# Optimization experiments

Measured on AMD Instinct MI355X. Metric: run time of the kernel, lower is better.

Reference implementation:

```python
import jax, jax.numpy as jnp
import numpy as np

B, T, IN, OUT = 131072, 8, 128, 128


def setup_inputs() -> dict:
    key = jax.random.key(0)
    k1, k2, k3, k4 = jax.random.split(key, 4)
    x = jax.random.normal(k1, (B, IN), dtype=jnp.float32)
    types = jax.random.randint(k2, (B,), 0, T, dtype=jnp.int64)
    # xavier_uniform over (out, in) fan dims
    limit = float(np.sqrt(6.0 / (IN + OUT)))
    W = jax.random.uniform(k3, (T, OUT, IN), dtype=jnp.float32, minval=-limit, maxval=limit)
    b = jnp.zeros((T, OUT), dtype=jnp.float32)
    return {"x": x, "types": types, "W": W, "b": b}


def reference(x, types, W, b):
    # y[i] = W[types[i]] @ x[i] + b[types[i]]
    # Compute all-type projections [B, T, OUT], then select per-token type.
    # This avoids materializing the huge [B, OUT, IN] gathered weight tensor.
    y_all = jnp.einsum("bi,toi->bto", x, W)           # [B, T, OUT]
    y = jnp.take_along_axis(y_all, types[:, None, None].astype(jnp.int32), axis=1)[:, 0, :]
    return y + b[types]
```

## Files before the change

### kernel.cpp

```cpp
#include <hip/hip_runtime.h>
#include <hip/hip_bf16.h>


typedef __attribute__((ext_vector_type(8))) short bf16x8;
typedef __attribute__((ext_vector_type(4))) short short4v;
typedef __attribute__((ext_vector_type(4))) float f32x4;
typedef __attribute__((ext_vector_type(4))) float float4v;

static constexpr int kBT = 128;
static constexpr int kT  = 8;
static constexpr int kD  = 128;

__device__ __forceinline__ short f2bf(float f) {
  union { __hip_bfloat16 h; short u; } cv;
  cv.h = __float2bfloat16(f);
  return cv.u;
}

__global__ __launch_bounds__(256) void wconv_kernel(const float* __restrict__ W,
                                                    short* __restrict__ Wb) {
  const int i = (blockIdx.x * 256 + threadIdx.x) * 8;
  float4v a = *(const float4v*)(W + i);
  float4v b = *(const float4v*)(W + i + 4);
  bf16x8 r;
  r[0] = f2bf(a[0]); r[1] = f2bf(a[1]); r[2] = f2bf(a[2]); r[3] = f2bf(a[3]);
  r[4] = f2bf(b[0]); r[5] = f2bf(b[1]); r[6] = f2bf(b[2]); r[7] = f2bf(b[3]);
  *(bf16x8*)(Wb + i) = r;
}

__global__ __launch_bounds__(256, 4) void typed_linear_kernel(
    const float* __restrict__ x, const int* __restrict__ types,
    const short* __restrict__ Wb, const float* __restrict__ bias,
    float* __restrict__ y) {
  __shared__ short xb[kBT * kD];
  __shared__ int s_cnt[kT];
  __shared__ unsigned char s_list[kT][kBT];

  const int tid  = threadIdx.x;
  const int tok0 = blockIdx.x * kBT;

  const float* xg = x + (size_t)tok0 * kD;
  float4v xr[16];
#pragma unroll
  for (int i = 0; i < 16; ++i)
    xr[i] = *(const float4v*)(xg + i * 1024 + tid * 4);

  if (tid < kT) s_cnt[tid] = 0;
  __syncthreads();
  if (tid < kBT) {
    const int t = types[tok0 + tid];
    const int pos = atomicAdd(&s_cnt[t], 1);
    s_list[t][pos] = (unsigned char)tid;
  }

#pragma unroll
  for (int i = 0; i < 16; ++i) {
    const int f    = i * 1024 + tid * 4;
    const int row  = f >> 7;
    const int col  = f & 127;
    const int slot = (col >> 3) ^ (row & 7);
    short4v v;
    v[0] = f2bf(xr[i][0]); v[1] = f2bf(xr[i][1]);
    v[2] = f2bf(xr[i][2]); v[3] = f2bf(xr[i][3]);
    *(short4v*)(xb + row * kD + slot * 8 + (col & 7)) = v;
  }
  __syncthreads();

  const int w    = tid >> 6;
  const int lane = tid & 63;
  const int lr   = lane & 15;
  const int lg   = lane >> 4;

  for (int t = 0; t < kT; ++t) {
    const int cnt = s_cnt[t];
    if (cnt == 0) continue;

    bf16x8 bfr[2][4];
    const short* wrow = Wb + ((t * kD + w * 32 + lr) * kD);
#pragma unroll
    for (int c = 0; c < 2; ++c)
#pragma unroll
      for (int s = 0; s < 4; ++s)
        bfr[c][s] = *(const bf16x8*)(wrow + c * 16 * kD + s * 32 + lg * 8);

    const float bias0 = bias[t * kD + w * 32 + lr];
    const float bias1 = bias[t * kD + w * 32 + 16 + lr];

    for (int m0 = 0; m0 < cnt; m0 += 16) {
      int ia = m0 + lr;
      ia = ia < cnt ? ia : cnt - 1;
      const int row = s_list[t][ia];

      bf16x8 afr[4];
#pragma unroll
      for (int s = 0; s < 4; ++s) {
        const int slot = ((s << 2) + lg) ^ (row & 7);
        afr[s] = *(const bf16x8*)(xb + row * kD + slot * 8);
      }

      f32x4 acc0 = {0.f, 0.f, 0.f, 0.f};
      f32x4 acc1 = {0.f, 0.f, 0.f, 0.f};
#pragma unroll
      for (int s = 0; s < 4; ++s) {
        acc0 = __builtin_amdgcn_mfma_f32_16x16x32_bf16(afr[s], bfr[0][s], acc0, 0, 0, 0);
        acc1 = __builtin_amdgcn_mfma_f32_16x16x32_bf16(afr[s], bfr[1][s], acc1, 0, 0, 0);
      }

#pragma unroll
      for (int r = 0; r < 4; ++r) {
        const int rl = lg * 4 + r;
        if (m0 + rl < cnt) {
          float* yp = y + (size_t)(tok0 + s_list[t][m0 + rl]) * kD + w * 32 + lr;
          yp[0]  = acc0[r] + bias0;
          yp[16] = acc1[r] + bias1;
        }
      }
    }
  }
}

extern "C" void kernel_launch(void* const* d_in, const int* in_sizes, int n_in,
                              void* d_out, int out_size, void* d_ws, size_t ws_size,
                              hipStream_t stream) {
  const float* x     = (const float*)d_in[0];
  const int*   types = (const int*)d_in[1];
  const float* W     = (const float*)d_in[2];
  const float* bias  = (const float*)d_in[3];
  float*       y     = (float*)d_out;
  short*       Wb    = (short*)d_ws;

  const int n_tok = in_sizes[0] / kD;

  wconv_kernel<<<(kT * kD * kD) / (256 * 8), 256, 0, stream>>>(W, Wb);
  typed_linear_kernel<<<n_tok / kBT, 256, 0, stream>>>(x, types, Wb, bias, y);
}
```

Measured before the change: 142.3 us.

## Use 512-thread blocks of 64 tokens with 16 output columns per wave

The block now covers 64 tokens with 8 waves instead of 128 tokens with 4 waves. Each wave handles 16 output columns with one accumulator instead of 32 columns with two. Launch bounds ask for more resident waves per CU, and the smaller register and LDS footprint should raise occupancy and hide global-memory latency better. The cost is that bf16 weight fragments are reloaded for twice as many blocks, so weight traffic per token doubles. The empty-type skip is removed, so weight fragments are now loaded even for types with no tokens.

Measured after the change: 166.5 us. 17.0% more time.

```diff
diff --git a/kernel.cpp b/kernel.cpp
--- a/kernel.cpp
+++ b/kernel.cpp
@@ -7,9 +7,10 @@
 typedef __attribute__((ext_vector_type(4))) float f32x4;
 typedef __attribute__((ext_vector_type(4))) float float4v;
 
-static constexpr int kBT = 128;
-static constexpr int kT  = 8;
-static constexpr int kD  = 128;
+static constexpr int kBT      = 64;
+static constexpr int kT       = 8;
+static constexpr int kD       = 128;
+static constexpr int kThreads = 512;
 
 __device__ __forceinline__ short f2bf(float f) {
   union { __hip_bfloat16 h; short u; } cv;
@@ -28,7 +29,7 @@
   *(bf16x8*)(Wb + i) = r;
 }
 
-__global__ __launch_bounds__(256, 4) void typed_linear_kernel(
+__global__ __launch_bounds__(kThreads, 8) void typed_linear_kernel(
     const float* __restrict__ x, const int* __restrict__ types,
     const short* __restrict__ Wb, const float* __restrict__ bias,
     float* __restrict__ y) {
@@ -40,10 +41,10 @@
   const int tok0 = blockIdx.x * kBT;
 
   const float* xg = x + (size_t)tok0 * kD;
-  float4v xr[16];
+  float4v xr[4];
 #pragma unroll
-  for (int i = 0; i < 16; ++i)
-    xr[i] = *(const float4v*)(xg + i * 1024 + tid * 4);
+  for (int i = 0; i < 4; ++i)
+    xr[i] = *(const float4v*)(xg + i * (kThreads * 4) + tid * 4);
 
   if (tid < kT) s_cnt[tid] = 0;
   __syncthreads();
@@ -54,8 +55,8 @@
   }
 
 #pragma unroll
-  for (int i = 0; i < 16; ++i) {
-    const int f    = i * 1024 + tid * 4;
+  for (int i = 0; i < 4; ++i) {
+    const int f    = i * (kThreads * 4) + tid * 4;
     const int row  = f >> 7;
     const int col  = f & 127;
     const int slot = (col >> 3) ^ (row & 7);
@@ -71,20 +72,18 @@
   const int lr   = lane & 15;
   const int lg   = lane >> 4;
 
+  const short* wbase = Wb + (w * 16 + lr) * kD;
+
+#pragma unroll
   for (int t = 0; t < kT; ++t) {
     const int cnt = s_cnt[t];
-    if (cnt == 0) continue;
 
-    bf16x8 bfr[2][4];
-    const short* wrow = Wb + ((t * kD + w * 32 + lr) * kD);
+    bf16x8 bfr[4];
+    const short* wrow = wbase + t * kD * kD;
 #pragma unroll
-    for (int c = 0; c < 2; ++c)
-#pragma unroll
-      for (int s = 0; s < 4; ++s)
-        bfr[c][s] = *(const bf16x8*)(wrow + c * 16 * kD + s * 32 + lg * 8);
-
-    const float bias0 = bias[t * kD + w * 32 + lr];
-    const float bias1 = bias[t * kD + w * 32 + 16 + lr];
+    for (int s = 0; s < 4; ++s)
+      bfr[s] = *(const bf16x8*)(wrow + s * 32 + lg * 8);
+    const float bias0 = bias[t * kD + w * 16 + lr];
 
     for (int m0 = 0; m0 < cnt; m0 += 16) {
       int ia = m0 + lr;
@@ -98,21 +97,16 @@
         afr[s] = *(const bf16x8*)(xb + row * kD + slot * 8);
       }
 
-      f32x4 acc0 = {0.f, 0.f, 0.f, 0.f};
-      f32x4 acc1 = {0.f, 0.f, 0.f, 0.f};
+      f32x4 acc = {0.f, 0.f, 0.f, 0.f};
 #pragma unroll
-      for (int s = 0; s < 4; ++s) {
-        acc0 = __builtin_amdgcn_mfma_f32_16x16x32_bf16(afr[s], bfr[0][s], acc0, 0, 0, 0);
-        acc1 = __builtin_amdgcn_mfma_f32_16x16x32_bf16(afr[s], bfr[1][s], acc1, 0, 0, 0);
-      }
+      for (int s = 0; s < 4; ++s)
+        acc = __builtin_amdgcn_mfma_f32_16x16x32_bf16(afr[s], bfr[s], acc, 0, 0, 0);
 
 #pragma unroll
       for (int r = 0; r < 4; ++r) {
         const int rl = lg * 4 + r;
         if (m0 + rl < cnt) {
-          float* yp = y + (size_t)(tok0 + s_list[t][m0 + rl]) * kD + w * 32 + lr;
-          yp[0]  = acc0[r] + bias0;
-          yp[16] = acc1[r] + bias1;
+          y[(size_t)(tok0 + s_list[t][m0 + rl]) * kD + w * 16 + lr] = acc[r] + bias0;
         }
       }
     }
@@ -132,5 +126,5 @@
   const int n_tok = in_sizes[0] / kD;
 
   wconv_kernel<<<(kT * kD * kD) / (256 * 8), 256, 0, stream>>>(W, Wb);
-  typed_linear_kernel<<<n_tok / kBT, 256, 0, stream>>>(x, types, Wb, bias, y);
+  typed_linear_kernel<<<n_tok / kBT, kThreads, 0, stream>>>(x, types, Wb, bias, y);
 }
```
